# Kernel optimization log

Measured on AMD Instinct MI355X. Metric: run time of the kernel, lower is better.

## Reference

```python
import jax, jax.numpy as jnp
import numpy as np

N = 100000
E = 1600000
D_IN = 128
D_H = 128


def _sage_conv(x, src, dst, W_self, W_neigh, b, n_nodes):
    # mean aggregation over in-neighbors: dst receives from src
    gathered = x[src]                                        # [E, D]
    summed = jax.ops.segment_sum(gathered, dst, num_segments=n_nodes)  # [N, D]
    deg = jax.ops.segment_sum(jnp.ones((src.shape[0],), x.dtype), dst,
                              num_segments=n_nodes)          # [N]
    mean_neigh = summed / jnp.maximum(deg, 1.0)[:, None]     # zero-degree -> 0
    return x @ W_self + mean_neigh @ W_neigh + b


def setup_inputs() -> dict:
    key = jax.random.key(0)
    ks = jax.random.split(key, 9)
    s1 = 1.0 / np.sqrt(D_IN)
    s2 = 1.0 / np.sqrt(D_H)
    return {
        "in_feat": jax.random.normal(ks[0], (N, D_IN), jnp.float32),
        "W1_self": jax.random.uniform(ks[1], (D_IN, D_H), jnp.float32, -s1, s1),
        "W1_neigh": jax.random.uniform(ks[2], (D_IN, D_H), jnp.float32, -s1, s1),
        "b1": jnp.zeros((D_H,), jnp.float32),
        "W2_self": jax.random.uniform(ks[3], (D_H, D_H), jnp.float32, -s2, s2),
        "W2_neigh": jax.random.uniform(ks[4], (D_H, D_H), jnp.float32, -s2, s2),
        "b2": jnp.zeros((D_H,), jnp.float32),
        "src": jax.random.randint(ks[5], (E,), 0, N, jnp.int32),
        "dst": jax.random.randint(ks[6], (E,), 0, N, jnp.int32),
    }


def reference(in_feat, W1_self, W1_neigh, b1, W2_self, W2_neigh, b2, src, dst):
    h = _sage_conv(in_feat, src, dst, W1_self, W1_neigh, b1, N)
    h = jax.nn.relu(h)
    h = _sage_conv(h, src, dst, W2_self, W2_neigh, b2, N)
    return h
```

## Files before the change

kernel.cpp:

```cpp
#include <hip/hip_runtime.h>
#include <hip/hip_fp16.h>

#define D 128
#define NB_MAX 1024
#define CNT_BLOCKS 512
#define PV_CHUNK 6250
#define PV_CAP   6400
#define CS_CAP   5376

using f32x4  = __attribute__((ext_vector_type(4))) float;
using half8  = __attribute__((ext_vector_type(8))) _Float16;
using short8 = __attribute__((ext_vector_type(8))) short;

#define AS1(p) ((const __attribute__((address_space(1))) void*)(p))
#define AS3(p) ((__attribute__((address_space(3))) void*)(p))

#define FMA_MIX_LO(acc, dw, one) \
    asm("v_fma_mix_f32 %0, %1, %2, %0 op_sel:[0,0,0] op_sel_hi:[1,0,0]" \
        : "+v"(acc) : "v"(dw), "v"(one))
#define FMA_MIX_HI(acc, dw, one) \
    asm("v_fma_mix_f32 %0, %1, %2, %0 op_sel:[1,0,0] op_sel_hi:[1,0,0]" \
        : "+v"(acc) : "v"(dw), "v"(one))

__global__ void prep_k(const float* __restrict__ x, __half* __restrict__ y, int n4,
                       const float* __restrict__ W1s, const float* __restrict__ W1n,
                       const float* __restrict__ W2s, const float* __restrict__ W2n,
                       unsigned short* __restrict__ Wg1, unsigned short* __restrict__ Wg2,
                       const int* __restrict__ dst, int* __restrict__ bucket_counts,
                       int E, int nb, float* __restrict__ xpad) {
    __shared__ int hist[NB_MAX];
    int b = blockIdx.x;
    int t = threadIdx.x;
    if (b < CNT_BLOCKS) {
        if (b == 0 && t < 64) xpad[t] = 0.f;
        for (int i = t; i < nb; i += 256) hist[i] = 0;
        __syncthreads();
        for (int i = b * 256 + t; i < E; i += CNT_BLOCKS * 256)
            atomicAdd(&hist[dst[i] >> 8], 1);
        __syncthreads();
        for (int i = t; i < nb; i += 256) {
            int c = hist[i];
            if (c) atomicAdd(&bucket_counts[i], c);
        }
        return;
    }
    int wb = b - CNT_BLOCKS;
    if (wb < 256) {
        int sel = wb >> 7;
        int lb  = wb & 127;
        const float* Ws = sel ? W2s : W1s;
        const float* Wn = sel ? W2n : W1n;
        unsigned short* Wg = sel ? Wg2 : Wg1;
        int idx = lb * 256 + t;
        int col = idx >> 8;
        int k   = idx & 255;
        float v = (k < 128) ? Ws[k * D + col] : Wn[(k - 128) * D + col];
        _Float16 hv = (_Float16)v;
        _Float16 lv = (_Float16)(v - (float)hv);
        int kc = k >> 5, q = (k >> 3) & 3, j = k & 7;
        Wg[(((kc * 2 + 0) * 4 + q) * 128 + col) * 8 + j] = *(unsigned short*)&hv;
        Wg[(((kc * 2 + 1) * 4 + q) * 128 + col) * 8 + j] = *(unsigned short*)&lv;
        return;
    }
    int i = (b - CNT_BLOCKS - 256) * 256 + t;
    if (i < n4) {
        float4 v = *(const float4*)(x + (size_t)i * 4);
        __half2 h0 = __floats2half2_rn(v.x, v.y);
        __half2 h1 = __floats2half2_rn(v.z, v.w);
        __half2* o = (__half2*)(y + (size_t)i * 4);
        o[0] = h0; o[1] = h1;
    }
}

__global__ __launch_bounds__(256)
void partition_k(const int* __restrict__ src, const int* __restrict__ dst,
                 const int* __restrict__ bucket_counts, int* __restrict__ bucket_cursor,
                 unsigned* __restrict__ pairs, int E, int nb, int chunk) {
    __shared__ unsigned stage[PV_CAP];
    __shared__ int hist[NB_MAX];
    __shared__ int lbase[NB_MAX];
    __shared__ int gbase[NB_MAX];
    __shared__ long long shll[256];
    int t = threadIdx.x;
    int e0 = blockIdx.x * chunk;
    int e1 = min(E, e0 + chunk);
    for (int b = t; b < NB_MAX; b += 256) hist[b] = 0;
    __syncthreads();
    for (int i = e0 + t; i < e1; i += 256)
        atomicAdd(&hist[dst[i] >> 8], 1);
    __syncthreads();
    int t4 = t * 4;
    int gb[4], lb[4];
    long long tsum = 0;
    #pragma unroll
    for (int j = 0; j < 4; ++j) {
        gb[j] = bucket_counts[t4 + j];
        lb[j] = hist[t4 + j];
        tsum += ((long long)gb[j] << 32) | (unsigned)lb[j];
    }
    shll[t] = tsum;
    __syncthreads();
    for (int off = 1; off < 256; off <<= 1) {
        long long v = 0;
        if (t >= off) v = shll[t - off];
        __syncthreads();
        if (t >= off) shll[t] += v;
        __syncthreads();
    }
    long long ex = shll[t] - tsum;
    int ge = (int)(ex >> 32);
    int le = (int)(ex & 0xffffffffLL);
    #pragma unroll
    for (int j = 0; j < 4; ++j) {
        int bkt = t4 + j;
        lbase[bkt] = le;
        int c = lb[j];
        int g = ge;
        if (c) g += atomicAdd(&bucket_cursor[bkt], c);
        gbase[bkt] = g;
        hist[bkt] = 0;
        ge += gb[j];
        le += c;
    }
    __syncthreads();
    for (int i = e0 + t; i < e1; i += 256) {
        int dd = dst[i];
        int b = dd >> 8;
        int r = atomicAdd(&hist[b], 1);
        stage[lbase[b] + r] = ((unsigned)(dd & 255) << 17) | (unsigned)src[i];
    }
    __syncthreads();
    int g16 = t >> 4, sub = t & 15;
    for (int b = g16; b < nb; b += 16) {
        int c = hist[b];
        int l0 = lbase[b], g0 = gbase[b];
        for (int j = sub; j < c; j += 16)
            pairs[g0 + j] = stage[l0 + j];
    }
}

__global__ __launch_bounds__(256)
void build_csr_k(const unsigned* __restrict__ pairs,
                 const int* __restrict__ bucket_counts,
                 int2* __restrict__ offcnt,
                 int* __restrict__ edge_src, int N) {
    __shared__ int srcs[CS_CAP];
    __shared__ int hist[256];
    __shared__ int curs[256];
    __shared__ int sh[256];
    __shared__ int e0s, cnts;
    int t = threadIdx.x;
    int b = blockIdx.x;
    int t4 = t * 4;
    int g0 = bucket_counts[t4], g1 = bucket_counts[t4 + 1];
    int g2 = bucket_counts[t4 + 2], g3 = bucket_counts[t4 + 3];
    int gs = g0 + g1 + g2 + g3;
    sh[t] = gs;
    hist[t] = 0;
    __syncthreads();
    for (int off = 1; off < 256; off <<= 1) {
        int v = 0;
        if (t >= off) v = sh[t - off];
        __syncthreads();
        if (t >= off) sh[t] += v;
        __syncthreads();
    }
    if (t == (b >> 2)) {
        int ex = sh[t] - gs;
        int v[4] = {g0, g1, g2, g3};
        #pragma unroll
        for (int j = 0; j < 4; ++j)
            if (j < (b & 3)) ex += v[j];
        e0s = ex;
        cnts = v[b & 3];
    }
    __syncthreads();
    int e0 = e0s, cnt = cnts, e1 = e0 + cnt;
    for (int i = e0 + t; i < e1; i += 256)
        atomicAdd(&hist[pairs[i] >> 17], 1);
    __syncthreads();
    int c = hist[t];
    sh[t] = c;
    __syncthreads();
    for (int off = 1; off < 256; off <<= 1) {
        int v = 0;
        if (t >= off) v = sh[t - off];
        __syncthreads();
        if (t >= off) sh[t] += v;
        __syncthreads();
    }
    int excl = sh[t] - c;
    curs[t] = excl;
    int node = (b << 8) + t;
    if (node < N) offcnt[node] = make_int2(e0 + excl, c);
    __syncthreads();
    for (int i = e0 + t; i < e1; i += 256) {
        unsigned p = pairs[i];
        int pos = atomicAdd(&curs[p >> 17], 1);
        int s = (int)(p & 0x1FFFFu);
        if (pos < CS_CAP) srcs[pos] = s;
        else edge_src[e0 + pos] = s;
    }
    __syncthreads();
    int lim = min(cnt, CS_CAP);
    for (int i = t; i < lim; i += 256)
        edge_src[e0 + i] = srcs[i];
}

__global__ void aggregate_f16_k(const __half* __restrict__ x,
                                const int* __restrict__ edge_src,
                                const int2* __restrict__ offcnt,
                                __half* __restrict__ agg, int n) {
    int wid  = (blockIdx.x * blockDim.x + threadIdx.x) >> 6;
    int lane = threadIdx.x & 63;
    if (wid >= n) return;
    int sg  = lane >> 4;
    int sub = lane & 15;
    int2 oc = offcnt[wid];
    int start = oc.x;
    int cnt   = oc.y;
    float one = 1.0f;
    float acc[8] = {0.f, 0.f, 0.f, 0.f, 0.f, 0.f, 0.f, 0.f};
    for (int base = 0; base < cnt; base += 64) {
        int valid = min(64, cnt - base);
        int s = (lane < valid) ? edge_src[start + base + lane] : n;
        for (int k0 = 0; k0 < valid; k0 += 16) {
            float4 raw[4];
            #pragma unroll
            for (int u = 0; u < 4; ++u) {
                int row = __shfl(s, (k0 + 4 * u + sg) & 63);
                raw[u] = *(const float4*)(x + (size_t)row * D + sub * 8);
            }
            #pragma unroll
            for (int u = 0; u < 4; ++u) {
                const unsigned* dw = (const unsigned*)&raw[u];
                #pragma unroll
                for (int j = 0; j < 4; ++j) {
                    FMA_MIX_LO(acc[2 * j],     dw[j], one);
                    FMA_MIX_HI(acc[2 * j + 1], dw[j], one);
                }
            }
        }
    }
    #pragma unroll
    for (int j = 0; j < 8; ++j) {
        acc[j] += __shfl(acc[j], lane ^ 16);
        acc[j] += __shfl(acc[j], lane ^ 32);
    }
    if (sg == 0) {
        float inv = 1.0f / fmaxf((float)cnt, 1.0f);
        union { __half2 h2[4]; short8 s8; } u;
        #pragma unroll
        for (int j = 0; j < 4; ++j)
            u.h2[j] = __floats2half2_rn(acc[2 * j] * inv, acc[2 * j + 1] * inv);
        *(short8*)(agg + (size_t)wid * D + sub * 8) = u.s8;
    }
}

__global__ __launch_bounds__(512)
void mfma_gemm_k(const _Float16* __restrict__ A0, const _Float16* __restrict__ A1,
                 const unsigned short* __restrict__ Wg,
                 const float* __restrict__ bias,
                 float* __restrict__ C, __half* __restrict__ Ch,
                 int n, int out_mode) {
    __shared__ __align__(16) unsigned short lds_b[8192];
    int t = threadIdx.x;
    int w = t >> 6;
    int l = t & 63;
    int m = l & 15;
    int q = l >> 4;
    int r0 = blockIdx.x * 256 + w * 32;

    f32x4 acc[2][8];
    #pragma unroll
    for (int rt = 0; rt < 2; ++rt)
        #pragma unroll
        for (int ct = 0; ct < 8; ++ct)
            acc[rt][ct] = (f32x4){0.f, 0.f, 0.f, 0.f};

    for (int kc = 0; kc < 8; ++kc) {
        const unsigned short* gk = Wg + (size_t)kc * 8192;
        #pragma unroll
        for (int i = 0; i < 2; ++i) {
            int e = i * 512 + t;
            __builtin_amdgcn_global_load_lds(AS1(gk + e * 8), AS3(lds_b + e * 8), 16, 0, 0);
        }
        const _Float16* __restrict__ A = (kc < 4) ? A0 : A1;
        int ka = (kc & 3) * 32;
        half8 a[2];
        #pragma unroll
        for (int rt = 0; rt < 2; ++rt) {
            int row = r0 + rt * 16 + m;
            half8 v = (half8){0, 0, 0, 0, 0, 0, 0, 0};
            if (row < n) v = *(const half8*)(A + (size_t)row * D + ka + q * 8);
            a[rt] = v;
        }
        __syncthreads();

        #pragma unroll
        for (int ct = 0; ct < 8; ++ct) {
            half8 bh = *(const half8*)&lds_b[(size_t)(q * 128 + ct * 16 + m) * 8];
            half8 bl = *(const half8*)&lds_b[(size_t)((4 + q) * 128 + ct * 16 + m) * 8];
            #pragma unroll
            for (int rt = 0; rt < 2; ++rt) {
                acc[rt][ct] = __builtin_amdgcn_mfma_f32_16x16x32_f16(a[rt], bh, acc[rt][ct], 0, 0, 0);
                acc[rt][ct] = __builtin_amdgcn_mfma_f32_16x16x32_f16(a[rt], bl, acc[rt][ct], 0, 0, 0);
            }
        }
        __syncthreads();
    }

    #pragma unroll
    for (int ct = 0; ct < 8; ++ct) {
        int col = ct * 16 + m;
        float bb = bias[col];
        #pragma unroll
        for (int rt = 0; rt < 2; ++rt) {
            #pragma unroll
            for (int r = 0; r < 4; ++r) {
                int row = r0 + rt * 16 + q * 4 + r;
                if (row < n) {
                    float v = acc[rt][ct][r] + bb;
                    if (out_mode) {
                        v = fmaxf(v, 0.f);
                        Ch[(size_t)row * D + col] = __float2half(v);
                    } else {
                        C[(size_t)row * D + col] = v;
                    }
                }
            }
        }
    }
}

extern "C" void kernel_launch(void* const* d_in, const int* in_sizes, int n_in,
                              void* d_out, int out_size, void* d_ws, size_t ws_size,
                              hipStream_t stream) {
    const float* in_feat = (const float*)d_in[0];
    const float* W1s     = (const float*)d_in[1];
    const float* W1n     = (const float*)d_in[2];
    const float* b1      = (const float*)d_in[3];
    const float* W2s     = (const float*)d_in[4];
    const float* W2n     = (const float*)d_in[5];
    const float* b2      = (const float*)d_in[6];
    const int*   src     = (const int*)d_in[7];
    const int*   dst     = (const int*)d_in[8];

    const int N  = in_sizes[0] / D;
    const int E  = in_sizes[7];
    const int NB = (N + 255) >> 8;

    char* base = (char*)d_ws;
    size_t off = 0;
    __half* agg16 = (__half*)(base + off); off += (size_t)N * D * 2;
    __half* xh16  = (__half*)(base + off); off += ((size_t)N * D + D) * 2;
    int* edge_src = (int*)(base + off);    off += (size_t)E * 4;
    int2* offcnt  = (int2*)(base + off);   off += (size_t)(N + 2) * 8;
    unsigned short* Wg1 = (unsigned short*)(base + off); off += 65536 * 2;
    unsigned short* Wg2 = (unsigned short*)(base + off); off += 65536 * 2;
    int* bucket_counts = (int*)(base + off); off += NB_MAX * 4;
    int* bucket_cursor = (int*)(base + off); off += NB_MAX * 4;

    unsigned* pairs = (unsigned*)agg16;
    float* xpad = (float*)(xh16 + (size_t)N * D);

    const int n4 = (N * D) / 4;
    const int xb = (n4 + 255) / 256;
    const int pblk = (E + PV_CHUNK - 1) / PV_CHUNK;

    hipMemsetAsync(bucket_counts, 0, NB_MAX * 4 * 2, stream);

    hipLaunchKernelGGL(prep_k, dim3(CNT_BLOCKS + 256 + xb), dim3(256), 0, stream,
                       in_feat, xh16, n4, W1s, W1n, W2s, W2n, Wg1, Wg2,
                       dst, bucket_counts, E, NB, xpad);

    hipLaunchKernelGGL(partition_k, dim3(pblk), dim3(256), 0, stream,
                       src, dst, bucket_counts, bucket_cursor, pairs, E, NB, PV_CHUNK);
    hipLaunchKernelGGL(build_csr_k, dim3(NB), dim3(256), 0, stream,
                       pairs, bucket_counts, offcnt, edge_src, N);

    const dim3 aggGrid(((size_t)N * 64 + 255) / 256);
    const dim3 gemmGrid((N + 255) / 256);

    hipLaunchKernelGGL(aggregate_f16_k, aggGrid, dim3(256), 0, stream,
                       xh16, edge_src, offcnt, agg16, N);
    hipLaunchKernelGGL(mfma_gemm_k, gemmGrid, dim3(512), 0, stream,
                       (const _Float16*)xh16, (const _Float16*)agg16, Wg1, b1,
                       (float*)nullptr, xh16, N, 1);

    hipLaunchKernelGGL(aggregate_f16_k, aggGrid, dim3(256), 0, stream,
                       xh16, edge_src, offcnt, agg16, N);
    hipLaunchKernelGGL(mfma_gemm_k, gemmGrid, dim3(512), 0, stream,
                       (const _Float16*)xh16, (const _Float16*)agg16, Wg2, b2,
                       (float*)d_out, (__half*)nullptr, N, 0);
}
```

Before: 356.8 us.

## Build CSR via per-node global atomic counts and direct scatter

Replaces the two-pass bucketed partition plus in-shared-memory CSR build with a simpler scheme. Per-node degrees are counted with global atomics inside the prep kernel, offsets come from a per-bucket scan, and a scatter kernel places each edge using a global atomic cursor per node. This removes the intermediate pairs buffer and the staging passes, at the cost of many contended global atomics and random scattered writes. It also adds index clamping for robustness, and the edge order within each node becomes nondeterministic.

Result: slower. 464.5 us (+30.2%).

```diff
diff --git a/kernel.cpp b/kernel.cpp
--- a/kernel.cpp
+++ b/kernel.cpp
@@ -4,9 +4,6 @@
 #define D 128
 #define NB_MAX 1024
 #define CNT_BLOCKS 512
-#define PV_CHUNK 6250
-#define PV_CAP   6400
-#define CS_CAP   5376
 
 using f32x4  = __attribute__((ext_vector_type(4))) float;
 using half8  = __attribute__((ext_vector_type(8))) _Float16;
@@ -26,8 +23,9 @@
                        const float* __restrict__ W1s, const float* __restrict__ W1n,
                        const float* __restrict__ W2s, const float* __restrict__ W2n,
                        unsigned short* __restrict__ Wg1, unsigned short* __restrict__ Wg2,
-                       const int* __restrict__ dst, int* __restrict__ bucket_counts,
-                       int E, int nb, float* __restrict__ xpad) {
+                       const int* __restrict__ dst, int* __restrict__ counts,
+                       int* __restrict__ bucket_counts,
+                       int E, int nb, int N, float* __restrict__ xpad) {
     __shared__ int hist[NB_MAX];
     int b = blockIdx.x;
     int t = threadIdx.x;
@@ -35,8 +33,12 @@
         if (b == 0 && t < 64) xpad[t] = 0.f;
         for (int i = t; i < nb; i += 256) hist[i] = 0;
         __syncthreads();
-        for (int i = b * 256 + t; i < E; i += CNT_BLOCKS * 256)
-            atomicAdd(&hist[dst[i] >> 8], 1);
+        for (int i = b * 256 + t; i < E; i += CNT_BLOCKS * 256) {
+            int d = dst[i];
+            d = min(max(d, 0), N - 1);
+            atomicAdd(&hist[d >> 8], 1);
+            atomicAdd(&counts[d], 1);
+        }
         __syncthreads();
         for (int i = t; i < nb; i += 256) {
             int c = hist[i];
@@ -73,82 +75,11 @@
 }
 
 __global__ __launch_bounds__(256)
-void partition_k(const int* __restrict__ src, const int* __restrict__ dst,
-                 const int* __restrict__ bucket_counts, int* __restrict__ bucket_cursor,
-                 unsigned* __restrict__ pairs, int E, int nb, int chunk) {
-    __shared__ unsigned stage[PV_CAP];
-    __shared__ int hist[NB_MAX];
-    __shared__ int lbase[NB_MAX];
-    __shared__ int gbase[NB_MAX];
-    __shared__ long long shll[256];
-    int t = threadIdx.x;
-    int e0 = blockIdx.x * chunk;
-    int e1 = min(E, e0 + chunk);
-    for (int b = t; b < NB_MAX; b += 256) hist[b] = 0;
-    __syncthreads();
-    for (int i = e0 + t; i < e1; i += 256)
-        atomicAdd(&hist[dst[i] >> 8], 1);
-    __syncthreads();
-    int t4 = t * 4;
-    int gb[4], lb[4];
-    long long tsum = 0;
-    #pragma unroll
-    for (int j = 0; j < 4; ++j) {
-        gb[j] = bucket_counts[t4 + j];
-        lb[j] = hist[t4 + j];
-        tsum += ((long long)gb[j] << 32) | (unsigned)lb[j];
-    }
-    shll[t] = tsum;
-    __syncthreads();
-    for (int off = 1; off < 256; off <<= 1) {
-        long long v = 0;
-        if (t >= off) v = shll[t - off];
-        __syncthreads();
-        if (t >= off) shll[t] += v;
-        __syncthreads();
-    }
-    long long ex = shll[t] - tsum;
-    int ge = (int)(ex >> 32);
-    int le = (int)(ex & 0xffffffffLL);
-    #pragma unroll
-    for (int j = 0; j < 4; ++j) {
-        int bkt = t4 + j;
-        lbase[bkt] = le;
-        int c = lb[j];
-        int g = ge;
-        if (c) g += atomicAdd(&bucket_cursor[bkt], c);
-        gbase[bkt] = g;
-        hist[bkt] = 0;
-        ge += gb[j];
-        le += c;
-    }
-    __syncthreads();
-    for (int i = e0 + t; i < e1; i += 256) {
-        int dd = dst[i];
-        int b = dd >> 8;
-        int r = atomicAdd(&hist[b], 1);
-        stage[lbase[b] + r] = ((unsigned)(dd & 255) << 17) | (unsigned)src[i];
-    }
-    __syncthreads();
-    int g16 = t >> 4, sub = t & 15;
-    for (int b = g16; b < nb; b += 16) {
-        int c = hist[b];
-        int l0 = lbase[b], g0 = gbase[b];
-        for (int j = sub; j < c; j += 16)
-            pairs[g0 + j] = stage[l0 + j];
-    }
-}
-
-__global__ __launch_bounds__(256)
-void build_csr_k(const unsigned* __restrict__ pairs,
-                 const int* __restrict__ bucket_counts,
-                 int2* __restrict__ offcnt,
-                 int* __restrict__ edge_src, int N) {
-    __shared__ int srcs[CS_CAP];
-    __shared__ int hist[256];
-    __shared__ int curs[256];
+void offsets_k(int* __restrict__ counts_cursor,
+               const int* __restrict__ bucket_counts,
+               int2* __restrict__ offcnt, int N) {
     __shared__ int sh[256];
-    __shared__ int e0s, cnts;
+    __shared__ int e0s;
     int t = threadIdx.x;
     int b = blockIdx.x;
     int t4 = t * 4;
@@ -156,7 +87,6 @@
     int g2 = bucket_counts[t4 + 2], g3 = bucket_counts[t4 + 3];
     int gs = g0 + g1 + g2 + g3;
     sh[t] = gs;
-    hist[t] = 0;
     __syncthreads();
     for (int off = 1; off < 256; off <<= 1) {
         int v = 0;
@@ -172,14 +102,11 @@
         for (int j = 0; j < 4; ++j)
             if (j < (b & 3)) ex += v[j];
         e0s = ex;
-        cnts = v[b & 3];
     }
     __syncthreads();
-    int e0 = e0s, cnt = cnts, e1 = e0 + cnt;
-    for (int i = e0 + t; i < e1; i += 256)
-        atomicAdd(&hist[pairs[i] >> 17], 1);
-    __syncthreads();
-    int c = hist[t];
+    int e0 = e0s;
+    int node = (b << 8) + t;
+    int c = (node < N) ? counts_cursor[node] : 0;
     sh[t] = c;
     __syncthreads();
     for (int off = 1; off < 256; off <<= 1) {
@@ -190,21 +117,39 @@
         __syncthreads();
     }
     int excl = sh[t] - c;
-    curs[t] = excl;
-    int node = (b << 8) + t;
-    if (node < N) offcnt[node] = make_int2(e0 + excl, c);
-    __syncthreads();
-    for (int i = e0 + t; i < e1; i += 256) {
-        unsigned p = pairs[i];
-        int pos = atomicAdd(&curs[p >> 17], 1);
-        int s = (int)(p & 0x1FFFFu);
-        if (pos < CS_CAP) srcs[pos] = s;
-        else edge_src[e0 + pos] = s;
-    }
-    __syncthreads();
-    int lim = min(cnt, CS_CAP);
-    for (int i = t; i < lim; i += 256)
-        edge_src[e0 + i] = srcs[i];
+    if (node < N) {
+        int o = e0 + excl;
+        offcnt[node] = make_int2(o, c);
+        counts_cursor[node] = o;
+    }
+}
+
+__global__ __launch_bounds__(256)
+void scatter_k(const int* __restrict__ src, const int* __restrict__ dst,
+               int* __restrict__ cursor, int* __restrict__ edge_src, int E, int N) {
+    int i = (blockIdx.x * 256 + threadIdx.x) * 4;
+    if (i + 3 < E) {
+        int4 s4 = *(const int4*)(src + i);
+        int4 d4 = *(const int4*)(dst + i);
+        int c0 = min(max(d4.x, 0), N - 1);
+        int c1 = min(max(d4.y, 0), N - 1);
+        int c2 = min(max(d4.z, 0), N - 1);
+        int c3 = min(max(d4.w, 0), N - 1);
+        int p0 = min(atomicAdd(&cursor[c0], 1), E - 1);
+        int p1 = min(atomicAdd(&cursor[c1], 1), E - 1);
+        int p2 = min(atomicAdd(&cursor[c2], 1), E - 1);
+        int p3 = min(atomicAdd(&cursor[c3], 1), E - 1);
+        edge_src[p0] = s4.x;
+        edge_src[p1] = s4.y;
+        edge_src[p2] = s4.z;
+        edge_src[p3] = s4.w;
+    } else {
+        for (; i < E; ++i) {
+            int c = min(max(dst[i], 0), N - 1);
+            int p = min(atomicAdd(&cursor[c], 1), E - 1);
+            edge_src[p] = src[i];
+        }
+    }
 }
 
 __global__ void aggregate_f16_k(const __half* __restrict__ x,
@@ -224,6 +169,7 @@
     for (int base = 0; base < cnt; base += 64) {
         int valid = min(64, cnt - base);
         int s = (lane < valid) ? edge_src[start + base + lane] : n;
+        s = min(max(s, 0), n);
         for (int k0 = 0; k0 < valid; k0 += 16) {
             float4 raw[4];
             #pragma unroll
@@ -358,26 +304,25 @@
     int2* offcnt  = (int2*)(base + off);   off += (size_t)(N + 2) * 8;
     unsigned short* Wg1 = (unsigned short*)(base + off); off += 65536 * 2;
     unsigned short* Wg2 = (unsigned short*)(base + off); off += 65536 * 2;
+    int* counts        = (int*)(base + off); off += (size_t)N * 4;
     int* bucket_counts = (int*)(base + off); off += NB_MAX * 4;
-    int* bucket_cursor = (int*)(base + off); off += NB_MAX * 4;
-
-    unsigned* pairs = (unsigned*)agg16;
+
     float* xpad = (float*)(xh16 + (size_t)N * D);
 
     const int n4 = (N * D) / 4;
     const int xb = (n4 + 255) / 256;
-    const int pblk = (E + PV_CHUNK - 1) / PV_CHUNK;
-
-    hipMemsetAsync(bucket_counts, 0, NB_MAX * 4 * 2, stream);
+    const int sblk = (E / 4 + 255) / 256;
+
+    hipMemsetAsync(counts, 0, (size_t)N * 4 + NB_MAX * 4, stream);
 
     hipLaunchKernelGGL(prep_k, dim3(CNT_BLOCKS + 256 + xb), dim3(256), 0, stream,
                        in_feat, xh16, n4, W1s, W1n, W2s, W2n, Wg1, Wg2,
-                       dst, bucket_counts, E, NB, xpad);
-
-    hipLaunchKernelGGL(partition_k, dim3(pblk), dim3(256), 0, stream,
-                       src, dst, bucket_counts, bucket_cursor, pairs, E, NB, PV_CHUNK);
-    hipLaunchKernelGGL(build_csr_k, dim3(NB), dim3(256), 0, stream,
-                       pairs, bucket_counts, offcnt, edge_src, N);
+                       dst, counts, bucket_counts, E, NB, N, xpad);
+
+    hipLaunchKernelGGL(offsets_k, dim3(NB), dim3(256), 0, stream,
+                       counts, bucket_counts, offcnt, N);
+    hipLaunchKernelGGL(scatter_k, dim3(sblk), dim3(256), 0, stream,
+                       src, dst, counts, edge_src, E, N);
 
     const dim3 aggGrid(((size_t)N * 64 + 255) / 256);
     const dim3 gemmGrid((N + 255) / 256);
```

## Fuse CSR build with first-layer aggregation and drop LDS staging in partition

Applied to the files above, without the earlier changes.

Partition now scatters pairs straight to global memory instead of staging them in LDS. It uses CNT_BLOCKS blocks and writes into the output buffer so that agg16 stays free. The CSR build and the first-layer mean aggregation are merged into one 1024-thread kernel per 256-node bucket, which reads neighbour sources from LDS. This removes a kernel launch and a global round trip of edge_src for layer 1. In exchange, the fused kernel has only about 391 large blocks, which may limit parallelism and occupancy during aggregation, and the partition writes to global memory are now uncoalesced.

New measurement: 378.3 us. +6.0%, slower.

```diff
diff --git a/kernel.cpp b/kernel.cpp
--- a/kernel.cpp
+++ b/kernel.cpp
@@ -4,9 +4,7 @@
 #define D 128
 #define NB_MAX 1024
 #define CNT_BLOCKS 512
-#define PV_CHUNK 6250
-#define PV_CAP   6400
-#define CS_CAP   5376
+#define CS_CAP 5376
 
 using f32x4  = __attribute__((ext_vector_type(4))) float;
 using half8  = __attribute__((ext_vector_type(8))) _Float16;
@@ -76,9 +74,7 @@
 void partition_k(const int* __restrict__ src, const int* __restrict__ dst,
                  const int* __restrict__ bucket_counts, int* __restrict__ bucket_cursor,
                  unsigned* __restrict__ pairs, int E, int nb, int chunk) {
-    __shared__ unsigned stage[PV_CAP];
     __shared__ int hist[NB_MAX];
-    __shared__ int lbase[NB_MAX];
     __shared__ int gbase[NB_MAX];
     __shared__ long long shll[256];
     int t = threadIdx.x;
@@ -109,92 +105,90 @@
     }
     long long ex = shll[t] - tsum;
     int ge = (int)(ex >> 32);
-    int le = (int)(ex & 0xffffffffLL);
     #pragma unroll
     for (int j = 0; j < 4; ++j) {
         int bkt = t4 + j;
-        lbase[bkt] = le;
         int c = lb[j];
         int g = ge;
         if (c) g += atomicAdd(&bucket_cursor[bkt], c);
         gbase[bkt] = g;
         hist[bkt] = 0;
         ge += gb[j];
-        le += c;
     }
     __syncthreads();
     for (int i = e0 + t; i < e1; i += 256) {
         int dd = dst[i];
         int b = dd >> 8;
         int r = atomicAdd(&hist[b], 1);
-        stage[lbase[b] + r] = ((unsigned)(dd & 255) << 17) | (unsigned)src[i];
-    }
-    __syncthreads();
-    int g16 = t >> 4, sub = t & 15;
-    for (int b = g16; b < nb; b += 16) {
-        int c = hist[b];
-        int l0 = lbase[b], g0 = gbase[b];
-        for (int j = sub; j < c; j += 16)
-            pairs[g0 + j] = stage[l0 + j];
-    }
-}
-
-__global__ __launch_bounds__(256)
-void build_csr_k(const unsigned* __restrict__ pairs,
-                 const int* __restrict__ bucket_counts,
-                 int2* __restrict__ offcnt,
-                 int* __restrict__ edge_src, int N) {
+        pairs[gbase[b] + r] = ((unsigned)(dd & 255) << 17) | (unsigned)src[i];
+    }
+}
+
+__global__ __launch_bounds__(1024)
+void csr_agg_k(const __half* __restrict__ x, const unsigned* __restrict__ pairs,
+               const int* __restrict__ bucket_counts,
+               int2* __restrict__ offcnt, int* __restrict__ edge_src,
+               __half* __restrict__ agg, int n) {
     __shared__ int srcs[CS_CAP];
+    __shared__ int sh[256];
     __shared__ int hist[256];
     __shared__ int curs[256];
-    __shared__ int sh[256];
+    __shared__ int soff[256];
+    __shared__ int scnt[256];
     __shared__ int e0s, cnts;
     int t = threadIdx.x;
     int b = blockIdx.x;
-    int t4 = t * 4;
-    int g0 = bucket_counts[t4], g1 = bucket_counts[t4 + 1];
-    int g2 = bucket_counts[t4 + 2], g3 = bucket_counts[t4 + 3];
-    int gs = g0 + g1 + g2 + g3;
-    sh[t] = gs;
-    hist[t] = 0;
+    int g0 = 0, g1 = 0, g2 = 0, g3 = 0, gs = 0;
+    if (t < 256) {
+        int t4 = t * 4;
+        g0 = bucket_counts[t4];     g1 = bucket_counts[t4 + 1];
+        g2 = bucket_counts[t4 + 2]; g3 = bucket_counts[t4 + 3];
+        gs = g0 + g1 + g2 + g3;
+        sh[t] = gs;
+        hist[t] = 0;
+    }
     __syncthreads();
     for (int off = 1; off < 256; off <<= 1) {
         int v = 0;
-        if (t >= off) v = sh[t - off];
-        __syncthreads();
-        if (t >= off) sh[t] += v;
+        if (t >= off && t < 256) v = sh[t - off];
+        __syncthreads();
+        if (t >= off && t < 256) sh[t] += v;
         __syncthreads();
     }
     if (t == (b >> 2)) {
         int ex = sh[t] - gs;
-        int v[4] = {g0, g1, g2, g3};
+        int vv[4] = {g0, g1, g2, g3};
         #pragma unroll
         for (int j = 0; j < 4; ++j)
-            if (j < (b & 3)) ex += v[j];
+            if (j < (b & 3)) ex += vv[j];
         e0s = ex;
-        cnts = v[b & 3];
+        cnts = vv[b & 3];
     }
     __syncthreads();
     int e0 = e0s, cnt = cnts, e1 = e0 + cnt;
-    for (int i = e0 + t; i < e1; i += 256)
+    for (int i = e0 + t; i < e1; i += 1024)
         atomicAdd(&hist[pairs[i] >> 17], 1);
     __syncthreads();
-    int c = hist[t];
-    sh[t] = c;
+    int c = 0;
+    if (t < 256) { c = hist[t]; sh[t] = c; }
     __syncthreads();
     for (int off = 1; off < 256; off <<= 1) {
         int v = 0;
-        if (t >= off) v = sh[t - off];
-        __syncthreads();
-        if (t >= off) sh[t] += v;
-        __syncthreads();
-    }
-    int excl = sh[t] - c;
-    curs[t] = excl;
-    int node = (b << 8) + t;
-    if (node < N) offcnt[node] = make_int2(e0 + excl, c);
-    __syncthreads();
-    for (int i = e0 + t; i < e1; i += 256) {
+        if (t >= off && t < 256) v = sh[t - off];
+        __syncthreads();
+        if (t >= off && t < 256) sh[t] += v;
+        __syncthreads();
+    }
+    if (t < 256) {
+        int excl = sh[t] - c;
+        curs[t] = excl;
+        soff[t] = excl;
+        scnt[t] = c;
+        int node = (b << 8) + t;
+        if (node < n) offcnt[node] = make_int2(e0 + excl, c);
+    }
+    __syncthreads();
+    for (int i = e0 + t; i < e1; i += 1024) {
         unsigned p = pairs[i];
         int pos = atomicAdd(&curs[p >> 17], 1);
         int s = (int)(p & 0x1FFFFu);
@@ -203,8 +197,54 @@
     }
     __syncthreads();
     int lim = min(cnt, CS_CAP);
-    for (int i = t; i < lim; i += 256)
+    for (int i = t; i < lim; i += 1024)
         edge_src[e0 + i] = srcs[i];
+    int lane = t & 63, wv = t >> 6;
+    int sg = lane >> 4, sub = lane & 15;
+    float one = 1.0f;
+    for (int nl = wv; nl < 256; nl += 16) {
+        int node = (b << 8) + nl;
+        if (node >= n) break;
+        int lstart = soff[nl];
+        int cnt2 = scnt[nl];
+        float acc[8] = {0.f, 0.f, 0.f, 0.f, 0.f, 0.f, 0.f, 0.f};
+        for (int base = 0; base < cnt2; base += 64) {
+            int valid = min(64, cnt2 - base);
+            int ls = lstart + base + lane;
+            int s = n;
+            if (lane < valid) s = (ls < CS_CAP) ? srcs[ls] : edge_src[e0 + ls];
+            for (int k0 = 0; k0 < valid; k0 += 16) {
+                float4 raw[4];
+                #pragma unroll
+                for (int u = 0; u < 4; ++u) {
+                    int row = __shfl(s, (k0 + 4 * u + sg) & 63);
+                    raw[u] = *(const float4*)(x + (size_t)row * D + sub * 8);
+                }
+                #pragma unroll
+                for (int u = 0; u < 4; ++u) {
+                    const unsigned* dw = (const unsigned*)&raw[u];
+                    #pragma unroll
+                    for (int j = 0; j < 4; ++j) {
+                        FMA_MIX_LO(acc[2 * j],     dw[j], one);
+                        FMA_MIX_HI(acc[2 * j + 1], dw[j], one);
+                    }
+                }
+            }
+        }
+        #pragma unroll
+        for (int j = 0; j < 8; ++j) {
+            acc[j] += __shfl(acc[j], lane ^ 16);
+            acc[j] += __shfl(acc[j], lane ^ 32);
+        }
+        if (sg == 0) {
+            float inv = 1.0f / fmaxf((float)cnt2, 1.0f);
+            union { __half2 h2[4]; short8 s8; } u8;
+            #pragma unroll
+            for (int j = 0; j < 4; ++j)
+                u8.h2[j] = __floats2half2_rn(acc[2 * j] * inv, acc[2 * j + 1] * inv);
+            *(short8*)(agg + (size_t)node * D + sub * 8) = u8.s8;
+        }
+    }
 }
 
 __global__ void aggregate_f16_k(const __half* __restrict__ x,
@@ -361,12 +401,12 @@
     int* bucket_counts = (int*)(base + off); off += NB_MAX * 4;
     int* bucket_cursor = (int*)(base + off); off += NB_MAX * 4;
 
-    unsigned* pairs = (unsigned*)agg16;
+    unsigned* pairs = (unsigned*)d_out;
     float* xpad = (float*)(xh16 + (size_t)N * D);
 
     const int n4 = (N * D) / 4;
     const int xb = (n4 + 255) / 256;
-    const int pblk = (E + PV_CHUNK - 1) / PV_CHUNK;
+    const int chunk = (E + CNT_BLOCKS - 1) / CNT_BLOCKS;
 
     hipMemsetAsync(bucket_counts, 0, NB_MAX * 4 * 2, stream);
 
@@ -374,16 +414,14 @@
                        in_feat, xh16, n4, W1s, W1n, W2s, W2n, Wg1, Wg2,
                        dst, bucket_counts, E, NB, xpad);
 
-    hipLaunchKernelGGL(partition_k, dim3(pblk), dim3(256), 0, stream,
-                       src, dst, bucket_counts, bucket_cursor, pairs, E, NB, PV_CHUNK);
-    hipLaunchKernelGGL(build_csr_k, dim3(NB), dim3(256), 0, stream,
-                       pairs, bucket_counts, offcnt, edge_src, N);
-
+    hipLaunchKernelGGL(partition_k, dim3(CNT_BLOCKS), dim3(256), 0, stream,
+                       src, dst, bucket_counts, bucket_cursor, pairs, E, NB, chunk);
+
+    const dim3 gemmGrid((N + 255) / 256);
     const dim3 aggGrid(((size_t)N * 64 + 255) / 256);
-    const dim3 gemmGrid((N + 255) / 256);
-
-    hipLaunchKernelGGL(aggregate_f16_k, aggGrid, dim3(256), 0, stream,
-                       xh16, edge_src, offcnt, agg16, N);
+
+    hipLaunchKernelGGL(csr_agg_k, dim3(NB), dim3(1024), 0, stream,
+                       xh16, pairs, bucket_counts, offcnt, edge_src, agg16, N);
     hipLaunchKernelGGL(mfma_gemm_k, gemmGrid, dim3(512), 0, stream,
                        (const _Float16*)xh16, (const _Float16*)agg16, Wg1, b1,
                        (float*)nullptr, xh16, N, 1);
```
